# Kernel tuning notes

Hardware: AMD Instinct MI355X
Metric: run time of the kernel (lower is better)

The kernel has to match this reference:

```python
import jax, jax.numpy as jnp
import numpy as np

B = 1024
S_OUT, S_IN, D_IN = 30, 17, 3
H = 4
DKQ_I, DV_I, HID_I, OUT_I = 6, 8, 256, 64
DKQ_O, DV_O, HID_O = 64, 64, 1024
OUT_O = 36 * S_OUT  # 1080


def _mha(x, wq, bq, wk, bk, wv, bv, dkq):
    """Vectorized multi-head self-attention over all heads at once.
    x: [..., P, d_in]; wq/wk: [H, d_in, dkq]; wv: [H, d_in, dv].
    Returns context [..., H, P, dv] (matches torch stack+permute ordering)."""
    q = jnp.einsum('...pd,hdk->...hpk', x, wq) + bq[:, None, :]
    k = jnp.einsum('...pd,hdk->...hpk', x, wk) + bk[:, None, :]
    v = jnp.einsum('...pd,hdv->...hpv', x, wv) + bv[:, None, :]
    scores = jnp.einsum('...hpk,...hqk->...hpq', q, k) / jnp.sqrt(jnp.asarray(dkq, x.dtype))
    attn = jax.nn.softmax(scores, axis=-1)
    return jnp.einsum('...hpq,...hqv->...hpv', attn, v)


def _ml(ctx, w1, b1, w2, b2):
    """MultiHeadLinearLayer: per-head fc1+tanh (shared weights), concat heads, fc2.
    ctx: [..., H, P, dv] -> [..., out]."""
    lead = ctx.shape[:-3]
    flat = ctx.reshape(*lead, H, -1)            # [..., H, P*dv]
    h = jnp.tanh(flat @ w1 + b1)                # [..., H, hidden]
    h = h.reshape(*lead, -1)                    # [..., H*hidden]
    return h @ w2 + b2


def setup_inputs() -> dict:
    key = jax.random.key(0)
    ks = iter(jax.random.split(key, 32))
    n = lambda shape, s=0.05: jax.random.normal(next(ks), shape, dtype=jnp.float32) * s
    inp = {
        'x': jax.random.normal(next(ks), (B, S_OUT, S_IN, D_IN), dtype=jnp.float32),
        # inner multi-head attention (4 heads, stacked weights)
        'iwq': n((H, D_IN, DKQ_I)), 'ibq': n((H, DKQ_I)),
        'iwk': n((H, D_IN, DKQ_I)), 'ibk': n((H, DKQ_I)),
        'iwv': n((H, D_IN, DV_I)),  'ibv': n((H, DV_I)),
        # inner MultiHeadLinearLayer
        'iw1': n((S_IN * DV_I, HID_I)), 'ib1': n((HID_I,)),
        'iw2': n((H * HID_I, OUT_I)),   'ib2': n((OUT_I,)),
        # outer multi-head attention
        'owq': n((H, OUT_I, DKQ_O)), 'obq': n((H, DKQ_O)),
        'owk': n((H, OUT_I, DKQ_O)), 'obk': n((H, DKQ_O)),
        'owv': n((H, OUT_I, DV_O)),  'obv': n((H, DV_O)),
        # outer MultiHeadLinearLayer
        'ow1': n((S_OUT * DV_O, HID_O)), 'ob1': n((HID_O,)),
        'ow2': n((H * HID_O, OUT_O)),    'ob2': n((OUT_O,)),
    }
    return inp


def reference(x, iwq, ibq, iwk, ibk, iwv, ibv, iw1, ib1, iw2, ib2,
              owq, obq, owk, obk, owv, obv, ow1, ob1, ow2, ob2):
    b = x.shape[0]
    # Inner attention applied to all 30 outer positions at once (replaces python loop)
    ctx_i = _mha(x, iwq, ibq, iwk, ibk, iwv, ibv, DKQ_I)      # [B,30,H,17,8]
    seq = _ml(ctx_i, iw1, ib1, iw2, ib2)                       # [B,30,64]
    # Outer attention over the 30-step sequence
    ctx_o = _mha(seq, owq, obq, owk, obk, owv, obv, DKQ_O)     # [B,H,30,64]
    out = _ml(ctx_o, ow1, ob1, ow2, ob2)                       # [B,1080]
    return out.reshape(b, S_OUT, 12, 3)
```

## Files before the change

### kernel.cpp

```cpp
#include <hip/hip_runtime.h>


typedef _Float16 f16x8 __attribute__((ext_vector_type(8)));
typedef _Float16 f16x4 __attribute__((ext_vector_type(4)));
typedef float    f32x4 __attribute__((ext_vector_type(4)));
typedef float    f32x16 __attribute__((ext_vector_type(16)));

union F16x8u { f16x8 v; f16x4 q[2]; };

__device__ inline float tanh_fast(float x) {
    float ax = fabsf(x);
    float e  = __expf(2.0f * ax);
    float r  = 1.0f - 2.0f / (e + 1.0f);
    return copysignf(r, x);
}

__device__ inline f32x16 zero16() {
    f32x16 z;
    #pragma unroll
    for (int i = 0; i < 16; i++) z[i] = 0.f;
    return z;
}

__device__ inline void tcast_tile(
    const float* __restrict__ W, _Float16* __restrict__ Wt,
    int tileIdx, int nkx, int K, int N, int Kpad,
    _Float16 (*tile)[65], int t)
{
    const int kx = tileIdx % nkx, ny = tileIdx / nkx;
    const int k0 = kx * 64, n0 = ny * 64;
    for (int i = t; i < 4096; i += 256) {
        const int r = i >> 6, c = i & 63;
        const int k = k0 + r, n = n0 + c;
        float v = (k < K && n < N) ? W[(size_t)k * N + n] : 0.f;
        tile[c][r] = (_Float16)v;
    }
    __syncthreads();
    for (int i = t; i < 4096; i += 256) {
        const int r = i >> 6, c = i & 63;
        Wt[(size_t)(n0 + r) * Kpad + k0 + c] = tile[r][c];
    }
}

__global__ __launch_bounds__(256) void k_prep_all(
    const float* __restrict__ iwq, const float* __restrict__ ibq,
    const float* __restrict__ iwk, const float* __restrict__ ibk,
    const float* __restrict__ iwv, const float* __restrict__ ibv,
    const float* __restrict__ iw1, const float* __restrict__ iw2,
    const float* __restrict__ ow1, const float* __restrict__ ow2,
    const float* __restrict__ owq, const float* __restrict__ owk,
    const float* __restrict__ owv,
    _Float16* __restrict__ wqf, _Float16* __restrict__ wkf,
    _Float16* __restrict__ wvf,
    _Float16* __restrict__ iw1t, _Float16* __restrict__ iw2t,
    _Float16* __restrict__ ow1t, _Float16* __restrict__ ow2t,
    _Float16* __restrict__ owqt, _Float16* __restrict__ owkt,
    _Float16* __restrict__ owvt)
{
    __shared__ _Float16 tile[64][65];
    const int b = blockIdx.x, t = threadIdx.x;
    if (b == 0) {
        const float SC = 0.40824829046386307f;
        for (int i = t; i < 512; i += 256) {
            const int lanev = i >> 3, jj = i & 7;
            const int n = lanev & 31, grp = lanev >> 5;
            const int h = n >> 3, dk = n & 7;
            float q = 0.f, k = 0.f, v = 0.f;
            if (!grp) {
                if (jj < 3) {
                    if (dk < 6) { q = iwq[h*18 + jj*6 + dk] * SC; k = iwk[h*18 + jj*6 + dk]; }
                    v = iwv[h*24 + jj*8 + dk];
                } else if (jj == 3) {
                    if (dk < 6) { q = ibq[h*6 + dk] * SC; k = ibk[h*6 + dk]; }
                    v = ibv[h*8 + dk];
                }
            }
            wqf[i] = (_Float16)q; wkf[i] = (_Float16)k; wvf[i] = (_Float16)v;
        }
    } else if (b < 161) {
        const int idx = (b - 1) * 256 + t;
        if (idx < 40960) {
            const int n = idx / 160, kp = idx - n * 160;
            const int dv = kp / 20, p = kp - dv * 20;
            float v = (p < 17) ? iw1[(p*8 + dv) * 256 + n] : 0.f;
            iw1t[n * 160 + kp] = (_Float16)v;
        }
    } else if (b < 177) {
        tcast_tile(iw2, iw2t, b - 161, 16, 1024, 64, 1024, tile, t);
    } else if (b < 657) {
        tcast_tile(ow1, ow1t, b - 177, 30, 1920, 1024, 1920, tile, t);
    } else if (b < 1745) {
        tcast_tile(ow2, ow2t, b - 657, 64, 4096, 1080, 4096, tile, t);
    } else {
        const int s = b - 1745;
        const int mat = s >> 6, rem = s & 63;
        const int h = rem >> 4, blk = rem & 15;
        const int idx = blk * 256 + t;
        const int n = idx >> 6, k = idx & 63;
        const float* W = (mat == 0) ? owq : (mat == 1) ? owk : owv;
        _Float16* Wt   = (mat == 0) ? owqt : (mat == 1) ? owkt : owvt;
        Wt[h * 4096 + n * 64 + k] = (_Float16)W[h * 4096 + k * 64 + n];
    }
}

__global__ __launch_bounds__(256, 3) void k_inner_attn_mfma(
    const float* __restrict__ x,
    const _Float16* __restrict__ wqf, const _Float16* __restrict__ wkf,
    const _Float16* __restrict__ wvf,
    _Float16* __restrict__ flat)
{
    __shared__ __align__(16) _Float16 lds[4][5248];
    const int t = threadIdx.x, lane = t & 63, w = t >> 6;
    const int l31 = lane & 31, grp = lane >> 5;
    const int bs = blockIdx.x * 4 + w;
    _Float16* kq  = &lds[w][0];
    _Float16* qq  = &lds[w][1152];
    _Float16* vt  = &lds[w][2304];
    _Float16* pf  = &lds[w][3456];
    _Float16* fo2 = &lds[w][4608];

    f16x8 xf;
    #pragma unroll
    for (int i = 0; i < 8; i++) xf[i] = (_Float16)0.f;
    if (grp == 0 && l31 < 17) {
        const float* xr = x + (size_t)bs * 51 + l31 * 3;
        xf[0] = (_Float16)xr[0];
        xf[1] = (_Float16)xr[1];
        xf[2] = (_Float16)xr[2];
        xf[3] = (_Float16)1.0f;
    }
    const f16x8 wq8 = *(const f16x8*)&wqf[lane * 8];
    const f16x8 wk8 = *(const f16x8*)&wkf[lane * 8];
    const f16x8 wv8 = *(const f16x8*)&wvf[lane * 8];

    f32x16 kt = __builtin_amdgcn_mfma_f32_32x32x16_f16(wk8, xf, zero16(), 0, 0, 0);
    f32x16 qt = __builtin_amdgcn_mfma_f32_32x32x16_f16(wq8, xf, zero16(), 0, 0, 0);
    f32x16 vv = __builtin_amdgcn_mfma_f32_32x32x16_f16(xf, wv8, zero16(), 0, 0, 0);

    #pragma unroll
    for (int qd = 0; qd < 4; qd++) {
        const int base = 8 * qd + 4 * grp;
        f16x4 a, b, c;
        #pragma unroll
        for (int i = 0; i < 4; i++) {
            a[i] = (_Float16)kt[4*qd + i];
            b[i] = (_Float16)qt[4*qd + i];
            c[i] = (_Float16)vv[4*qd + i];
        }
        *(f16x4*)&kq[l31 * 36 + base] = a;
        *(f16x4*)&qq[l31 * 36 + base] = b;
        *(f16x4*)&vt[l31 * 36 + base] = c;
    }

    #pragma unroll
    for (int h = 0; h < 4; h++) {
        F16x8u ka, qb;
        #pragma unroll
        for (int i = 0; i < 8; i++) { ka.v[i] = (_Float16)0.f; qb.v[i] = (_Float16)0.f; }
        if (grp == 0) {
            ka.q[0] = *(const f16x4*)&kq[l31 * 36 + h * 8];
            ka.q[1] = *(const f16x4*)&kq[l31 * 36 + h * 8 + 4];
            qb.q[0] = *(const f16x4*)&qq[l31 * 36 + h * 8];
            qb.q[1] = *(const f16x4*)&qq[l31 * 36 + h * 8 + 4];
        }
        f32x16 s = __builtin_amdgcn_mfma_f32_32x32x16_f16(ka.v, qb.v, zero16(), 0, 0, 0);

        float mx = -1e30f;
        #pragma unroll
        for (int r = 0; r < 16; r++) {
            const bool val = (r < 8) || (r == 8 && grp == 0);
            if (val) mx = fmaxf(mx, s[r]);
        }
        mx = fmaxf(mx, __shfl_xor(mx, 32));
        float e[16], sum = 0.f;
        #pragma unroll
        for (int r = 0; r < 16; r++) {
            const bool val = (r < 8) || (r == 8 && grp == 0);
            e[r] = val ? __expf(s[r] - mx) : 0.f;
            sum += e[r];
        }
        sum += __shfl_xor(sum, 32);
        const float inv = __builtin_amdgcn_rcpf(sum);
        #pragma unroll
        for (int qd = 0; qd < 4; qd++) {
            f16x4 pk;
            #pragma unroll
            for (int i = 0; i < 4; i++) pk[i] = (_Float16)(e[4*qd + i] * inv);
            *(f16x4*)&pf[l31 * 36 + 8 * qd + 4 * grp] = pk;
        }

        F16x8u pa1, pa2, vb1, vb2;
        pa1.q[0] = *(const f16x4*)&pf[l31 * 36 + grp * 8];
        pa1.q[1] = *(const f16x4*)&pf[l31 * 36 + grp * 8 + 4];
        pa2.q[0] = *(const f16x4*)&pf[l31 * 36 + 16 + grp * 8];
        pa2.q[1] = *(const f16x4*)&pf[l31 * 36 + 16 + grp * 8 + 4];
        const int vr = (h * 8 + (l31 & 7)) * 36;
        vb1.q[0] = *(const f16x4*)&vt[vr + grp * 8];
        vb1.q[1] = *(const f16x4*)&vt[vr + grp * 8 + 4];
        vb2.q[0] = *(const f16x4*)&vt[vr + 16 + grp * 8];
        vb2.q[1] = *(const f16x4*)&vt[vr + 16 + grp * 8 + 4];
        f32x16 c = __builtin_amdgcn_mfma_f32_32x32x16_f16(pa1.v, vb1.v, zero16(), 0, 0, 0);
        c = __builtin_amdgcn_mfma_f32_32x32x16_f16(pa2.v, vb2.v, c, 0, 0, 0);

        if (l31 < 8) {
            #pragma unroll
            for (int qd = 0; qd < 4; qd++) {
                const int jb = 8 * qd + 4 * grp;
                if (jb < 20) {
                    f16x4 ck;
                    #pragma unroll
                    for (int i = 0; i < 4; i++) ck[i] = (_Float16)c[4*qd + i];
                    *(f16x4*)&fo2[h * 160 + l31 * 20 + jb] = ck;
                }
            }
        }
    }

    _Float16* fg = flat + (size_t)bs * 640;
    *(f16x8*)&fg[lane * 8] = *(const f16x8*)&fo2[lane * 8];
    if (lane < 16)
        *(f16x8*)&fg[512 + lane * 8] = *(const f16x8*)&fo2[512 + lane * 8];
}

__global__ __launch_bounds__(256) void k_inner_ml_mfma(
    const _Float16* __restrict__ flat,
    const _Float16* __restrict__ iw1t,
    const _Float16* __restrict__ iw2t,
    const float* __restrict__ ib1, const float* __restrict__ ib2,
    float* __restrict__ seq)
{
    __shared__ __align__(16) _Float16 h1l[32][1032];
    float* red = (float*)&h1l[0][0];
    const int t = threadIdx.x, lane = t & 63, w = t >> 6;
    const int q = lane >> 4, ml = lane & 15;
    const int m0  = blockIdx.x * 128;
    const int bs0 = blockIdx.x * 32;

    for (int p = 0; p < 2; p++) {
        f32x4 acc[4][4];
        #pragma unroll
        for (int mi = 0; mi < 4; mi++)
            #pragma unroll
            for (int ni = 0; ni < 4; ni++) acc[mi][ni] = (f32x4){0.f,0.f,0.f,0.f};
        for (int ks = 0; ks < 5; ks++) {
            const int k = ks * 32 + q * 8;
            f16x8 a[4], b[4];
            #pragma unroll
            for (int mi = 0; mi < 4; mi++)
                a[mi] = *(const f16x8*)&flat[(size_t)(m0 + p*64 + mi*16 + ml) * 160 + k];
            #pragma unroll
            for (int ni = 0; ni < 4; ni++)
                b[ni] = *(const f16x8*)&iw1t[(size_t)(w*64 + ni*16 + ml) * 160 + k];
            #pragma unroll
            for (int mi = 0; mi < 4; mi++)
                #pragma unroll
                for (int ni = 0; ni < 4; ni++)
                    acc[mi][ni] = __builtin_amdgcn_mfma_f32_16x16x32_f16(a[mi], b[ni], acc[mi][ni], 0, 0, 0);
        }
        #pragma unroll
        for (int mi = 0; mi < 4; mi++)
            #pragma unroll
            for (int ni = 0; ni < 4; ni++)
                #pragma unroll
                for (int r = 0; r < 4; r++) {
                    const int row = p*64 + mi*16 + q*4 + r;
                    const int col = w*64 + ni*16 + ml;
                    const int bs_l = row >> 2, h = row & 3;
                    h1l[bs_l][h*256 + col] = (_Float16)tanh_fast(acc[mi][ni][r] + ib1[col]);
                }
    }
    __syncthreads();

    f32x4 a2[2][4];
    #pragma unroll
    for (int mi = 0; mi < 2; mi++)
        #pragma unroll
        for (int ni = 0; ni < 4; ni++) a2[mi][ni] = (f32x4){0.f,0.f,0.f,0.f};
    for (int ks = 0; ks < 8; ks++) {
        const int k = w * 256 + ks * 32 + q * 8;
        f16x8 a[2], b[4];
        #pragma unroll
        for (int mi = 0; mi < 2; mi++)
            a[mi] = *(const f16x8*)&h1l[mi*16 + ml][k];
        #pragma unroll
        for (int ni = 0; ni < 4; ni++)
            b[ni] = *(const f16x8*)&iw2t[(size_t)(ni*16 + ml) * 1024 + k];
        #pragma unroll
        for (int mi = 0; mi < 2; mi++)
            #pragma unroll
            for (int ni = 0; ni < 4; ni++)
                a2[mi][ni] = __builtin_amdgcn_mfma_f32_16x16x32_f16(a[mi], b[ni], a2[mi][ni], 0, 0, 0);
    }
    __syncthreads();
    #pragma unroll
    for (int mi = 0; mi < 2; mi++)
        #pragma unroll
        for (int ni = 0; ni < 4; ni++)
            #pragma unroll
            for (int r = 0; r < 4; r++) {
                const int row = mi*16 + q*4 + r;
                const int col = ni*16 + ml;
                red[(size_t)w*2048 + row*64 + col] = a2[mi][ni][r];
            }
    __syncthreads();
    for (int i = t; i < 2048; i += 256) {
        const int row = i >> 6, col = i & 63;
        float s = red[i] + red[2048 + i] + red[4096 + i] + red[6144 + i] + ib2[col];
        seq[(size_t)(bs0 + row) * 64 + col] = s;
    }
}

__device__ inline void oa_proj_rows(
    const _Float16 (*seqf)[72], const _Float16* __restrict__ wt,
    const float* __restrict__ bias, _Float16 (*dst)[72], int q, int ml)
{
    f32x4 acc[2][4];
    #pragma unroll
    for (int mi = 0; mi < 2; mi++)
        #pragma unroll
        for (int ni = 0; ni < 4; ni++) acc[mi][ni] = (f32x4){0.f,0.f,0.f,0.f};
    #pragma unroll
    for (int k0 = 0; k0 < 64; k0 += 32) {
        f16x8 a[2], bb[4];
        #pragma unroll
        for (int mi = 0; mi < 2; mi++) a[mi] = *(const f16x8*)&seqf[mi*16 + ml][k0 + q*8];
        #pragma unroll
        for (int ni = 0; ni < 4; ni++) bb[ni] = *(const f16x8*)&wt[(size_t)(ni*16 + ml)*64 + k0 + q*8];
        #pragma unroll
        for (int mi = 0; mi < 2; mi++)
            #pragma unroll
            for (int ni = 0; ni < 4; ni++)
                acc[mi][ni] = __builtin_amdgcn_mfma_f32_16x16x32_f16(a[mi], bb[ni], acc[mi][ni], 0, 0, 0);
    }
    #pragma unroll
    for (int ni = 0; ni < 4; ni++) {
        const float bi = bias[ni*16 + ml];
        #pragma unroll
        for (int mi = 0; mi < 2; mi++)
            #pragma unroll
            for (int r = 0; r < 4; r++)
                dst[mi*16 + q*4 + r][ni*16 + ml] = (_Float16)(acc[mi][ni][r] + bi);
    }
}

__device__ inline void oa_proj_t(
    const _Float16 (*seqf)[72], const _Float16* __restrict__ wt,
    const float* __restrict__ bias, _Float16 (*dstT)[40], int q, int ml)
{
    f32x4 acc[2][4];
    #pragma unroll
    for (int mi = 0; mi < 2; mi++)
        #pragma unroll
        for (int ni = 0; ni < 4; ni++) acc[mi][ni] = (f32x4){0.f,0.f,0.f,0.f};
    #pragma unroll
    for (int k0 = 0; k0 < 64; k0 += 32) {
        f16x8 a[2], bb[4];
        #pragma unroll
        for (int mi = 0; mi < 2; mi++) a[mi] = *(const f16x8*)&seqf[mi*16 + ml][k0 + q*8];
        #pragma unroll
        for (int ni = 0; ni < 4; ni++) bb[ni] = *(const f16x8*)&wt[(size_t)(ni*16 + ml)*64 + k0 + q*8];
        #pragma unroll
        for (int mi = 0; mi < 2; mi++)
            #pragma unroll
            for (int ni = 0; ni < 4; ni++)
                acc[mi][ni] = __builtin_amdgcn_mfma_f32_16x16x32_f16(a[mi], bb[ni], acc[mi][ni], 0, 0, 0);
    }
    #pragma unroll
    for (int ni = 0; ni < 4; ni++) {
        const float bi = bias[ni*16 + ml];
        #pragma unroll
        for (int mi = 0; mi < 2; mi++)
            #pragma unroll
            for (int r = 0; r < 4; r++)
                dstT[ni*16 + ml][mi*16 + q*4 + r] = (_Float16)(acc[mi][ni][r] + bi);
    }
}

__global__ __launch_bounds__(256) void k_outer_attn_mfma(
    const float* __restrict__ seq,
    const _Float16* __restrict__ owqt,
    const _Float16* __restrict__ owkt,
    const _Float16* __restrict__ owvt,
    const float* __restrict__ obq, const float* __restrict__ obk,
    const float* __restrict__ obv,
    _Float16* __restrict__ ctxo)
{
    __shared__ __align__(16) _Float16 seqf[32][72];
    __shared__ __align__(16) _Float16 qf[4][32][72];
    __shared__ __align__(16) _Float16 kf[4][32][72];
    __shared__ __align__(16) _Float16 vt[4][64][40];
    __shared__ __align__(16) _Float16 pf[4][32][40];
    const int t = threadIdx.x, lane = t & 63, w = t >> 6;
    const int q = lane >> 4, ml = lane & 15;
    const int b = blockIdx.x;

    const float* sb = seq + (size_t)b * 1920;
    for (int i = t; i < 2048; i += 256) {
        const int row = i >> 6, col = i & 63;
        seqf[row][col] = (_Float16)(row < 30 ? sb[row*64 + col] : 0.0f);
    }
    __syncthreads();

    oa_proj_rows(seqf, owqt + w*4096, obq + w*64, qf[w], q, ml);
    oa_proj_rows(seqf, owkt + w*4096, obk + w*64, kf[w], q, ml);
    oa_proj_t   (seqf, owvt + w*4096, obv + w*64, vt[w], q, ml);
    __syncthreads();

    f32x4 sc[2][2];
    #pragma unroll
    for (int mi = 0; mi < 2; mi++)
        #pragma unroll
        for (int ni = 0; ni < 2; ni++) sc[mi][ni] = (f32x4){0.f,0.f,0.f,0.f};
    #pragma unroll
    for (int k0 = 0; k0 < 64; k0 += 32) {
        f16x8 aq[2], bk[2];
        #pragma unroll
        for (int mi = 0; mi < 2; mi++) aq[mi] = *(const f16x8*)&qf[w][mi*16 + ml][k0 + q*8];
        #pragma unroll
        for (int ni = 0; ni < 2; ni++) bk[ni] = *(const f16x8*)&kf[w][ni*16 + ml][k0 + q*8];
        #pragma unroll
        for (int mi = 0; mi < 2; mi++)
            #pragma unroll
            for (int ni = 0; ni < 2; ni++)
                sc[mi][ni] = __builtin_amdgcn_mfma_f32_16x16x32_f16(aq[mi], bk[ni], sc[mi][ni], 0, 0, 0);
    }

    const bool maskhi = (ml >= 14);
    #pragma unroll
    for (int mi = 0; mi < 2; mi++) {
        #pragma unroll
        for (int r = 0; r < 4; r++) {
            const float s0 = sc[mi][0][r] * 0.125f;
            const float s1 = maskhi ? -1e30f : sc[mi][1][r] * 0.125f;
            float mx = fmaxf(s0, s1);
            #pragma unroll
            for (int off = 1; off < 16; off <<= 1) mx = fmaxf(mx, __shfl_xor(mx, off, 64));
            const float e0 = __expf(s0 - mx);
            const float e1 = __expf(s1 - mx);
            float sm = e0 + e1;
            #pragma unroll
            for (int off = 1; off < 16; off <<= 1) sm += __shfl_xor(sm, off, 64);
            const float inv = 1.0f / sm;
            pf[w][mi*16 + q*4 + r][ml]      = (_Float16)(e0 * inv);
            pf[w][mi*16 + q*4 + r][16 + ml] = (_Float16)(e1 * inv);
        }
    }
    __syncthreads();

    f16x8 ap[2], bv[4];
    #pragma unroll
    for (int mi = 0; mi < 2; mi++) ap[mi] = *(const f16x8*)&pf[w][mi*16 + ml][q*8];
    #pragma unroll
    for (int ni = 0; ni < 4; ni++) bv[ni] = *(const f16x8*)&vt[w][ni*16 + ml][q*8];
    f32x4 oa[2][4];
    #pragma unroll
    for (int mi = 0; mi < 2; mi++)
        #pragma unroll
        for (int ni = 0; ni < 4; ni++) {
            oa[mi][ni] = (f32x4){0.f,0.f,0.f,0.f};
            oa[mi][ni] = __builtin_amdgcn_mfma_f32_16x16x32_f16(ap[mi], bv[ni], oa[mi][ni], 0, 0, 0);
        }

    _Float16* co = ctxo + (size_t)(b*4 + w) * 1920;
    #pragma unroll
    for (int mi = 0; mi < 2; mi++)
        #pragma unroll
        for (int r = 0; r < 4; r++) {
            const int row = mi*16 + q*4 + r;
            if (row < 30) {
                #pragma unroll
                for (int ni = 0; ni < 4; ni++)
                    co[row*64 + ni*16 + ml] = (_Float16)oa[mi][ni][r];
            }
        }
}

__global__ __launch_bounds__(256) void k_outer_fc1_mfma(
    const _Float16* __restrict__ ctxo,
    const _Float16* __restrict__ ow1t,
    const float* __restrict__ ob1,
    _Float16* __restrict__ hout)
{
    __shared__ float red[2][64][65];
    const int t = threadIdx.x, lane = t & 63, w = t >> 6;
    const int q = lane >> 4, ml = lane & 15;
    const int mh = w >> 1, kh = w & 1;
    const int Mb = (blockIdx.x >> 4) * 128;
    const int M0 = Mb + mh * 64;
    const int N0 = (blockIdx.x & 15) * 64;
    const int kk0 = kh * 960 + q * 8;
    f32x4 acc[4][4];
    #pragma unroll
    for (int mi = 0; mi < 4; mi++)
        #pragma unroll
        for (int ni = 0; ni < 4; ni++) acc[mi][ni] = (f32x4){0.f,0.f,0.f,0.f};
    f16x8 a[2][4], b[2][4];
    #pragma unroll
    for (int mi = 0; mi < 4; mi++)
        a[0][mi] = *(const f16x8*)&ctxo[(size_t)(M0 + mi*16 + ml) * 1920 + kk0];
    #pragma unroll
    for (int ni = 0; ni < 4; ni++)
        b[0][ni] = *(const f16x8*)&ow1t[(size_t)(N0 + ni*16 + ml) * 1920 + kk0];
    #pragma unroll
    for (int ks = 0; ks < 30; ks++) {
        const int cur = ks & 1, nxt = cur ^ 1;
        if (ks < 29) {
            const int kn = kk0 + (ks + 1) * 32;
            #pragma unroll
            for (int mi = 0; mi < 4; mi++)
                a[nxt][mi] = *(const f16x8*)&ctxo[(size_t)(M0 + mi*16 + ml) * 1920 + kn];
            #pragma unroll
            for (int ni = 0; ni < 4; ni++)
                b[nxt][ni] = *(const f16x8*)&ow1t[(size_t)(N0 + ni*16 + ml) * 1920 + kn];
        }
        #pragma unroll
        for (int mi = 0; mi < 4; mi++)
            #pragma unroll
            for (int ni = 0; ni < 4; ni++)
                acc[mi][ni] = __builtin_amdgcn_mfma_f32_16x16x32_f16(a[cur][mi], b[cur][ni], acc[mi][ni], 0, 0, 0);
    }
    if (kh == 1) {
        #pragma unroll
        for (int mi = 0; mi < 4; mi++)
            #pragma unroll
            for (int ni = 0; ni < 4; ni++)
                #pragma unroll
                for (int r = 0; r < 4; r++)
                    red[mh][mi*16 + q*4 + r][ni*16 + ml] = acc[mi][ni][r];
    }
    __syncthreads();
    if (kh == 0) {
        #pragma unroll
        for (int mi = 0; mi < 4; mi++)
            #pragma unroll
            for (int ni = 0; ni < 4; ni++)
                #pragma unroll
                for (int r = 0; r < 4; r++)
                    red[mh][mi*16 + q*4 + r][ni*16 + ml] += acc[mi][ni][r];
    }
    __syncthreads();
    for (int i = t; i < 8192; i += 256) {
        const int row = i >> 6, col = i & 63;
        const float s = red[row >> 6][row & 63][col] + ob1[N0 + col];
        hout[(size_t)(Mb + row) * 1024 + N0 + col] = (_Float16)tanh_fast(s);
    }
}

__global__ __launch_bounds__(256) void k_outer_fc2_mfma(
    const _Float16* __restrict__ hout,
    const _Float16* __restrict__ ow2t,
    float* __restrict__ part)
{
    __shared__ float red[4][32][65];
    const int t = threadIdx.x, lane = t & 63, w = t >> 6;
    const int q = lane >> 4, ml = lane & 15;
    const int bid = blockIdx.x;
    const int kc = bid & 3;
    const int rest = bid >> 2;
    const int M0 = (rest / 17) * 32;
    const int N0 = (rest % 17) * 64;
    const int kk0 = kc * 1024 + w * 256 + q * 8;
    f32x4 acc[2][4];
    #pragma unroll
    for (int mi = 0; mi < 2; mi++)
        #pragma unroll
        for (int ni = 0; ni < 4; ni++) acc[mi][ni] = (f32x4){0.f,0.f,0.f,0.f};
    f16x8 a[2][2], b[2][4];
    #pragma unroll
    for (int mi = 0; mi < 2; mi++)
        a[0][mi] = *(const f16x8*)&hout[(size_t)(M0 + mi*16 + ml) * 4096 + kk0];
    #pragma unroll
    for (int ni = 0; ni < 4; ni++)
        b[0][ni] = *(const f16x8*)&ow2t[(size_t)(N0 + ni*16 + ml) * 4096 + kk0];
    #pragma unroll
    for (int ks = 0; ks < 8; ks++) {
        const int cur = ks & 1, nxt = cur ^ 1;
        if (ks < 7) {
            const int kn = kk0 + (ks + 1) * 32;
            #pragma unroll
            for (int mi = 0; mi < 2; mi++)
                a[nxt][mi] = *(const f16x8*)&hout[(size_t)(M0 + mi*16 + ml) * 4096 + kn];
            #pragma unroll
            for (int ni = 0; ni < 4; ni++)
                b[nxt][ni] = *(const f16x8*)&ow2t[(size_t)(N0 + ni*16 + ml) * 4096 + kn];
        }
        #pragma unroll
        for (int mi = 0; mi < 2; mi++)
            #pragma unroll
            for (int ni = 0; ni < 4; ni++)
                acc[mi][ni] = __builtin_amdgcn_mfma_f32_16x16x32_f16(a[cur][mi], b[cur][ni], acc[mi][ni], 0, 0, 0);
    }
    #pragma unroll
    for (int mi = 0; mi < 2; mi++)
        #pragma unroll
        for (int ni = 0; ni < 4; ni++)
            #pragma unroll
            for (int r = 0; r < 4; r++)
                red[w][mi*16 + q*4 + r][ni*16 + ml] = acc[mi][ni][r];
    __syncthreads();
    for (int i = t; i < 2048; i += 256) {
        const int row = i >> 6, col = i & 63;
        const int n = N0 + col;
        if (n < 1080) {
            const float s = red[0][row][col] + red[1][row][col] + red[2][row][col] + red[3][row][col];
            part[(size_t)kc * 1105920 + (size_t)(M0 + row) * 1080 + n] = s;
        }
    }
}

__global__ __launch_bounds__(256) void k_fc2_reduce(
    const float* __restrict__ part, const float* __restrict__ ob2,
    float* __restrict__ out)
{
    const int idx = blockIdx.x * 256 + threadIdx.x;
    if (idx >= 1105920) return;
    const int n = idx % 1080;
    out[idx] = part[idx] + part[1105920 + idx] + part[2211840 + idx]
             + part[3317760 + idx] + ob2[n];
}

extern "C" void kernel_launch(void* const* d_in, const int* in_sizes, int n_in,
                              void* d_out, int out_size, void* d_ws, size_t ws_size,
                              hipStream_t stream) {
    const float* x   = (const float*)d_in[0];
    const float* iwq = (const float*)d_in[1];
    const float* ibq = (const float*)d_in[2];
    const float* iwk = (const float*)d_in[3];
    const float* ibk = (const float*)d_in[4];
    const float* iwv = (const float*)d_in[5];
    const float* ibv = (const float*)d_in[6];
    const float* iw1 = (const float*)d_in[7];
    const float* ib1 = (const float*)d_in[8];
    const float* iw2 = (const float*)d_in[9];
    const float* ib2 = (const float*)d_in[10];
    const float* owq = (const float*)d_in[11];
    const float* obq = (const float*)d_in[12];
    const float* owk = (const float*)d_in[13];
    const float* obk = (const float*)d_in[14];
    const float* owv = (const float*)d_in[15];
    const float* obv = (const float*)d_in[16];
    const float* ow1 = (const float*)d_in[17];
    const float* ob1 = (const float*)d_in[18];
    const float* ow2 = (const float*)d_in[19];
    const float* ob2 = (const float*)d_in[20];

    char* ws = (char*)d_ws;
    _Float16* iw1t   = (_Float16*)(ws + 0);
    _Float16* wqf    = (_Float16*)(ws + 98304);
    _Float16* wkf    = (_Float16*)(ws + 99328);
    _Float16* wvf    = (_Float16*)(ws + 100352);
    _Float16* iw2t   = (_Float16*)(ws + 163840);
    _Float16* ow1t   = (_Float16*)(ws + 294912);
    _Float16* ow2t   = (_Float16*)(ws + 4227072);
    _Float16* flat   = (_Float16*)(ws + 13139968);
    float*    seq    = (float*)   (ws + 52461568);
    _Float16* owqt   = (_Float16*)(ws + 60325888);
    _Float16* owkt   = (_Float16*)(ws + 60358656);
    _Float16* owvt   = (_Float16*)(ws + 60391424);
    _Float16* ctxo   = (_Float16*)(ws + 13139968);
    float*    part2  = (float*)   (ws + 13139968);
    _Float16* houtb  = (_Float16*)(ws + 40000000);
    float*    out    = (float*)d_out;

    k_prep_all       <<<dim3(1937), dim3(256), 0, stream>>>(
        iwq, ibq, iwk, ibk, iwv, ibv, iw1, iw2, ow1, ow2, owq, owk, owv,
        wqf, wkf, wvf, iw1t, iw2t, ow1t, ow2t, owqt, owkt, owvt);
    k_inner_attn_mfma<<<dim3(7680), dim3(256), 0, stream>>>(x, wqf, wkf, wvf, flat);
    k_inner_ml_mfma  <<<dim3(960),  dim3(256), 0, stream>>>(flat, iw1t, iw2t, ib1, ib2, seq);
    k_outer_attn_mfma<<<dim3(1024), dim3(256), 0, stream>>>(seq, owqt, owkt, owvt, obq, obk, obv, ctxo);
    k_outer_fc1_mfma <<<dim3(512),  dim3(256), 0, stream>>>(ctxo, ow1t, ob1, houtb);
    k_outer_fc2_mfma <<<dim3(2176), dim3(256), 0, stream>>>(houtb, ow2t, part2);
    k_fc2_reduce     <<<dim3(4320), dim3(256), 0, stream>>>(part2, ob2, out);
}
```

Before: 338.1 us.

## Stage outer fc1 tiles in LDS via direct global-to-LDS loads, drop split-K reduction

The outer fc1 GEMM kernel stops loading A/B fragments straight from global memory into registers with a split-K wave layout. It now stages 128x32 A and 64x32 B tiles into shared memory with global_load_lds. Each wave computes a 64x32 output sub-tile over the full K, which removes the shared-memory cross-wave reduction. The aim is to cut redundant global traffic and the reduction cost, at the price of single-buffered loads with two barriers per k-step and no prefetch overlap.

```diff
diff --git a/kernel.cpp b/kernel.cpp
--- a/kernel.cpp
+++ b/kernel.cpp
@@ -7,6 +7,13 @@
 typedef float    f32x16 __attribute__((ext_vector_type(16)));
 
 union F16x8u { f16x8 v; f16x4 q[2]; };
+
+typedef __attribute__((address_space(1))) const unsigned int as1_u32;
+typedef __attribute__((address_space(3))) unsigned int as3_u32;
+
+__device__ inline void gl_lds16(const _Float16* g, _Float16* l) {
+    __builtin_amdgcn_global_load_lds((as1_u32*)g, (as3_u32*)l, 16, 0, 0);
+}
 
 __device__ inline float tanh_fast(float x) {
     float ax = fabsf(x);
@@ -481,68 +488,61 @@
     const float* __restrict__ ob1,
     _Float16* __restrict__ hout)
 {
-    __shared__ float red[2][64][65];
+    __shared__ __align__(16) _Float16 At[128][32];
+    __shared__ __align__(16) _Float16 Bt[64][32];
     const int t = threadIdx.x, lane = t & 63, w = t >> 6;
     const int q = lane >> 4, ml = lane & 15;
-    const int mh = w >> 1, kh = w & 1;
-    const int Mb = (blockIdx.x >> 4) * 128;
-    const int M0 = Mb + mh * 64;
-    const int N0 = (blockIdx.x & 15) * 64;
-    const int kk0 = kh * 960 + q * 8;
-    f32x4 acc[4][4];
+    const int M0 = (int)(blockIdx.x >> 4) * 128;
+    const int N0 = (int)(blockIdx.x & 15) * 64;
+    const int wm = (w >> 1) * 64, wn = (w & 1) * 32;
+
+    const int lrow = lane >> 2;
+    const int lcol = (lane & 3) * 8;
+    const _Float16* gA0 = ctxo + (size_t)(M0 + w*32 + lrow) * 1920 + lcol;
+    const _Float16* gA1 = gA0 + (size_t)16 * 1920;
+    const _Float16* gB0 = ow1t + (size_t)(N0 + w*16 + lrow) * 1920 + lcol;
+    _Float16* lA0 = &At[w*32][0];
+    _Float16* lA1 = &At[w*32 + 16][0];
+    _Float16* lB0 = &Bt[w*16][0];
+
+    f32x4 acc[4][2];
     #pragma unroll
     for (int mi = 0; mi < 4; mi++)
         #pragma unroll
-        for (int ni = 0; ni < 4; ni++) acc[mi][ni] = (f32x4){0.f,0.f,0.f,0.f};
-    f16x8 a[2][4], b[2][4];
-    #pragma unroll
-    for (int mi = 0; mi < 4; mi++)
-        a[0][mi] = *(const f16x8*)&ctxo[(size_t)(M0 + mi*16 + ml) * 1920 + kk0];
-    #pragma unroll
-    for (int ni = 0; ni < 4; ni++)
-        b[0][ni] = *(const f16x8*)&ow1t[(size_t)(N0 + ni*16 + ml) * 1920 + kk0];
-    #pragma unroll
-    for (int ks = 0; ks < 30; ks++) {
-        const int cur = ks & 1, nxt = cur ^ 1;
-        if (ks < 29) {
-            const int kn = kk0 + (ks + 1) * 32;
-            #pragma unroll
-            for (int mi = 0; mi < 4; mi++)
-                a[nxt][mi] = *(const f16x8*)&ctxo[(size_t)(M0 + mi*16 + ml) * 1920 + kn];
-            #pragma unroll
-            for (int ni = 0; ni < 4; ni++)
-                b[nxt][ni] = *(const f16x8*)&ow1t[(size_t)(N0 + ni*16 + ml) * 1920 + kn];
-        }
+        for (int ni = 0; ni < 2; ni++) acc[mi][ni] = (f32x4){0.f,0.f,0.f,0.f};
+
+    for (int ks = 0; ks < 60; ks++) {
+        const int k0 = ks * 32;
+        gl_lds16(gA0 + k0, lA0);
+        gl_lds16(gA1 + k0, lA1);
+        gl_lds16(gB0 + k0, lB0);
+        __syncthreads();
+        f16x8 a[4], b[2];
         #pragma unroll
         for (int mi = 0; mi < 4; mi++)
-            #pragma unroll
-            for (int ni = 0; ni < 4; ni++)
-                acc[mi][ni] = __builtin_amdgcn_mfma_f32_16x16x32_f16(a[cur][mi], b[cur][ni], acc[mi][ni], 0, 0, 0);
-    }
-    if (kh == 1) {
+            a[mi] = *(const f16x8*)&At[wm + mi*16 + ml][q*8];
+        #pragma unroll
+        for (int ni = 0; ni < 2; ni++)
+            b[ni] = *(const f16x8*)&Bt[wn + ni*16 + ml][q*8];
         #pragma unroll
         for (int mi = 0; mi < 4; mi++)
             #pragma unroll
-            for (int ni = 0; ni < 4; ni++)
-                #pragma unroll
-                for (int r = 0; r < 4; r++)
-                    red[mh][mi*16 + q*4 + r][ni*16 + ml] = acc[mi][ni][r];
-    }
-    __syncthreads();
-    if (kh == 0) {
+            for (int ni = 0; ni < 2; ni++)
+                acc[mi][ni] = __builtin_amdgcn_mfma_f32_16x16x32_f16(a[mi], b[ni], acc[mi][ni], 0, 0, 0);
+        __syncthreads();
+    }
+
+    #pragma unroll
+    for (int ni = 0; ni < 2; ni++) {
+        const int col = N0 + wn + ni*16 + ml;
+        const float bias = ob1[col];
         #pragma unroll
         for (int mi = 0; mi < 4; mi++)
             #pragma unroll
-            for (int ni = 0; ni < 4; ni++)
-                #pragma unroll
-                for (int r = 0; r < 4; r++)
-                    red[mh][mi*16 + q*4 + r][ni*16 + ml] += acc[mi][ni][r];
-    }
-    __syncthreads();
-    for (int i = t; i < 8192; i += 256) {
-        const int row = i >> 6, col = i & 63;
-        const float s = red[row >> 6][row & 63][col] + ob1[N0 + col];
-        hout[(size_t)(Mb + row) * 1024 + N0 + col] = (_Float16)tanh_fast(s);
+            for (int r = 0; r < 4; r++) {
+                const int row = M0 + wm + mi*16 + q*4 + r;
+                hout[(size_t)row * 1024 + col] = (_Float16)tanh_fast(acc[mi][ni][r] + bias);
+            }
     }
 }
 
```

After: 317.3 us. 6.2% less time.
